# Optimization experiments

Hardware: AMD Instinct MI355X
Metric: run time of the kernel (lower is better)

Reference implementation:

```python
import jax, jax.numpy as jnp
import numpy as np

B = 128
IN = 256
NLVL = 6
KLVL = 3
CH = 4
C = 4 * CH * CH          # 64 channels per node
OU = 8                   # out_filter_siz_u
OV = 8                   # out_filter_siz_v
NK = 2 ** KLVL           # 8 leaf nodes per axis
W_SCALE = 1.0 / 16.0     # ~1/sqrt(2*2*C) so 7 stacked relu-convs stay numerically sane


def setup_inputs() -> dict:
    key = jax.random.key(0)
    ks = jax.random.split(key, 2 * NLVL + 4)
    fx = IN // 2 ** NLVL  # 4: input patch filter size
    inp = {}
    inp["in_data"] = jax.random.normal(ks[0], (B, IN, IN, 1), jnp.float32)
    inp["in_filter"] = jax.random.normal(ks[1], (fx, fx, 1, C), jnp.float32) * W_SCALE
    inp["in_bias"] = jnp.zeros((C,), jnp.float32)
    i = 2
    for lvl in range(1, NLVL + 1):
        n = 2 ** min(lvl, KLVL)  # node grid: grows to 2^klvl then stays
        inp[f"f{lvl}"] = jax.random.normal(ks[i], (n, n, 2, 2, C, C), jnp.float32) * W_SCALE
        inp[f"b{lvl}"] = jnp.zeros((n, n, C), jnp.float32)
        i += 1
    inp["Wd"] = jax.random.normal(ks[i], (NK, NK, 2, C, OU * OV), jnp.float32) * W_SCALE
    return inp


def _node_conv(x, w, b):
    # x: [Nu,Nv,B,H,W,C]; w: [Nu,Nv,2,2,C,C]; 2x2 stride-2 VALID conv per node
    Nu, Nv, Bn, H, W, Cc = x.shape
    xr = x.reshape(Nu, Nv, Bn, H // 2, 2, W // 2, 2, Cc)
    y = jnp.einsum('uvbhxwyc,uvxyco->uvbhwo', xr, w)
    return jax.nn.relu(y + b[:, :, None, None, None, :])


def _forward(in_data, in_filter, in_bias, fs, bs, Wd):
    Bn = in_data.shape[0]
    fx, fy = in_filter.shape[0], in_filter.shape[1]
    # input interp conv: stride == kernel -> non-overlapping patch GEMM
    xr = in_data[..., 0].reshape(Bn, in_data.shape[1] // fx, fx, in_data.shape[2] // fy, fy)
    x = jax.nn.relu(jnp.einsum('bxpyq,pqc->bxyc', xr, in_filter[:, :, 0, :]) + in_bias)
    x = x[None, None]  # [1,1,B,2^nlvl,2^nlvl,C] node grid
    for lvl in range(1, NLVL + 1):
        if lvl <= KLVL:
            # children (itu,itv) read parent (itu//2, itv//2)
            x = jnp.repeat(jnp.repeat(x, 2, axis=0), 2, axis=1)
        x = _node_conv(x, fs[lvl - 1], bs[lvl - 1])
    feats = x[:, :, :, 0, 0, :]  # [NK,NK,B,C]; spatial is 1x1 at level nlvl
    out = jnp.einsum('uvbc,uvrck->uvbrk', feats, Wd)  # r in {real, imag}
    out = out.reshape(NK, NK, Bn, 2, OU, OV)
    out = jnp.transpose(out, (2, 0, 4, 1, 5, 3))  # [B,itu,ou,itv,ov,2]
    return out.reshape(Bn, NK * OU, NK * OV, 2)


def reference(in_data, in_filter, in_bias, f1, b1, f2, b2, f3, b3, f4, b4, f5, b5, f6, b6, Wd):
    fs = (f1, f2, f3, f4, f5, f6)
    bs = (b1, b2, b3, b4, b5, b6)
    return _forward(in_data, in_filter, in_bias, fs, bs, Wd)
```

## Files before the change

kernel.cpp:

```cpp
#include <hip/hip_runtime.h>
#include <hip/hip_bf16.h>
#include <cstdint>
#include <cstddef>


typedef __attribute__((ext_vector_type(8))) short short8;
typedef __attribute__((ext_vector_type(4))) float f32x4;
typedef unsigned short ushort_t;

static __device__ __forceinline__ float b2f(const __hip_bfloat16 x) {
    return __bfloat162float(x);
}
static __device__ __forceinline__ ushort_t f2bf(float x) {
    __hip_bfloat16 h = __float2bfloat16(x);
    ushort_t u;
    __builtin_memcpy(&u, &h, 2);
    return u;
}
static __device__ __forceinline__ void gl_lds16(const void* g, void* l) {
    __builtin_amdgcn_global_load_lds(
        (const __attribute__((address_space(1))) void*)g,
        (__attribute__((address_space(3))) void*)l, 16, 0, 0);
}

#define PREP_BLOCKS 2533

static __device__ __forceinline__ void prep_work(
    int gid, int isbf,
    const void* f1, const void* f2, const void* f3,
    const void* f4, const void* f5, const void* f6, const void* wdsrc,
    const void* b1, const void* b2, const void* b3,
    const void* b4, const void* b5, const void* b6,
    ushort_t* __restrict__ wbuf, ushort_t* __restrict__ wdbuf,
    float* __restrict__ bbuf)
{
    if (gid >= 648448) return;
    if (gid >= 630784) {
        const int bg = gid - 630784;
        const void* src; int base;
        if      (bg <   256) { src = b1; base = 0;     }
        else if (bg <  1280) { src = b2; base = 256;   }
        else if (bg <  5376) { src = b3; base = 1280;  }
        else if (bg <  9472) { src = b4; base = 5376;  }
        else if (bg < 13568) { src = b5; base = 9472;  }
        else                 { src = b6; base = 13568; }
        const int local = bg - base;
        bbuf[bg] = isbf ? b2f(((const __hip_bfloat16*)src)[local])
                        : ((const float*)src)[local];
        return;
    }
    if (gid >= 565248) {
        const int local = gid - 565248;
        const int lane = local & 63;
        const int slot = (local >> 6) & 15;
        const int site = local >> 10;
        const int ks2 = slot >> 3, nh = slot & 7, q = lane >> 4;
        const int n = nh * 16 + (lane & 15);
        const int r = n >> 6, kk = n & 63;
        const int cbase = ks2 * 32 + q * 8;
        ushort_t pk[8];
        if (isbf) {
            const ushort_t* s = (const ushort_t*)wdsrc;
            #pragma unroll
            for (int j = 0; j < 8; j++)
                pk[j] = s[(((size_t)(site * 2 + r) * 64 + cbase + j) * 64) + kk];
        } else {
            const float* s = (const float*)wdsrc;
            #pragma unroll
            for (int j = 0; j < 8; j++)
                pk[j] = f2bf(s[(((size_t)(site * 2 + r) * 64 + cbase + j) * 64) + kk]);
        }
        *(uint4*)&wdbuf[(size_t)local * 8] = *(uint4*)pk;
        return;
    }
    const void* fsrc; int base;
    if      (gid <   8192) { fsrc = f1; base = 0;      }
    else if (gid <  40960) { fsrc = f2; base = 8192;   }
    else if (gid < 172032) { fsrc = f3; base = 40960;  }
    else if (gid < 303104) { fsrc = f4; base = 172032; }
    else if (gid < 434176) { fsrc = f5; base = 303104; }
    else                   { fsrc = f6; base = 434176; }
    const int local = gid - base;
    const int lane = local & 63;
    const int slot = (local >> 6) & 7;
    const int sitetap = local >> 9;
    const int ks = slot >> 2, nh = slot & 3, q = lane >> 4;
    const int n = (lane & 15) + nh * 16;
    const int kbase = ks * 32 + q * 8;
    ushort_t pk[8];
    if (isbf) {
        const ushort_t* s = (const ushort_t*)fsrc + (size_t)sitetap * 4096;
        #pragma unroll
        for (int j = 0; j < 8; j++) pk[j] = s[(kbase + j) * 64 + n];
    } else {
        const float* s = (const float*)fsrc + (size_t)sitetap * 4096;
        #pragma unroll
        for (int j = 0; j < 8; j++) pk[j] = f2bf(s[(kbase + j) * 64 + n]);
    }
    *(uint4*)&wbuf[(size_t)gid * 8] = *(uint4*)pk;
}

static __device__ __forceinline__ void stage0_body(
    int blk, int isbf,
    const void* __restrict__ in_data, const void* __restrict__ filt,
    const void* __restrict__ bias, __hip_bfloat16* __restrict__ x0,
    int b_off)
{
    const int X  = blk & 63;
    const int bl = blk >> 6;
    const int bg = bl + b_off;

    __shared__ float sIn[4][256];
    __shared__ float sF[16][64];
    __shared__ float sB[64];

    const int t = threadIdx.x;
    const size_t srow = ((size_t)bg * 256 + (size_t)X * 4) * 256;

    if (isbf) {
        const __hip_bfloat16* src = (const __hip_bfloat16*)in_data + srow;
        #pragma unroll
        for (int i = 0; i < 4; i++) {
            int flat = i * 256 + t;
            int p = flat >> 8, col = flat & 255;
            sIn[p][col] = b2f(src[(size_t)p * 256 + col]);
        }
        const __hip_bfloat16* fsrc = (const __hip_bfloat16*)filt;
        #pragma unroll
        for (int i = 0; i < 4; i++) {
            int flat = i * 256 + t;
            sF[flat >> 6][flat & 63] = b2f(fsrc[flat]);
        }
        if (t < 64) sB[t] = b2f(((const __hip_bfloat16*)bias)[t]);
    } else {
        const float* src = (const float*)in_data + srow;
        const int p = t >> 6, c4 = (t & 63) * 4;
        *(float4*)&sIn[p][c4] = *(const float4*)(src + (size_t)p * 256 + c4);
        const float* fsrc = (const float*)filt;
        #pragma unroll
        for (int i = 0; i < 4; i++) {
            int flat = i * 256 + t;
            sF[flat >> 6][flat & 63] = fsrc[flat];
        }
        if (t < 64) sB[t] = ((const float*)bias)[t];
    }
    __syncthreads();

    const int ty = t >> 4;
    const int tc = t & 15;

    float acc[4][4];
    {
        const float4 bv = *(const float4*)&sB[tc * 4];
        #pragma unroll
        for (int yi = 0; yi < 4; yi++) {
            acc[yi][0] = bv.x; acc[yi][1] = bv.y;
            acc[yi][2] = bv.z; acc[yi][3] = bv.w;
        }
    }

    #pragma unroll
    for (int p = 0; p < 4; p++) {
        float4 rin[4], rf[4];
        #pragma unroll
        for (int yi = 0; yi < 4; yi++)
            rin[yi] = *(const float4*)&sIn[p][ty * 16 + yi * 4];
        #pragma unroll
        for (int q = 0; q < 4; q++)
            rf[q] = *(const float4*)&sF[p * 4 + q][tc * 4];
        #pragma unroll
        for (int yi = 0; yi < 4; yi++) {
            #pragma unroll
            for (int q = 0; q < 4; q++) {
                const float a = ((const float*)&rin[yi])[q];
                acc[yi][0] = fmaf(a, rf[q].x, acc[yi][0]);
                acc[yi][1] = fmaf(a, rf[q].y, acc[yi][1]);
                acc[yi][2] = fmaf(a, rf[q].z, acc[yi][2]);
                acc[yi][3] = fmaf(a, rf[q].w, acc[yi][3]);
            }
        }
    }

    ushort_t* dst = (ushort_t*)(x0 + ((size_t)bl * 64 + X) * 64 * 64);
    #pragma unroll
    for (int yi = 0; yi < 4; yi++) {
        uint2 pk;
        pk.x = (uint32_t)f2bf(fmaxf(acc[yi][0], 0.f))
             | ((uint32_t)f2bf(fmaxf(acc[yi][1], 0.f)) << 16);
        pk.y = (uint32_t)f2bf(fmaxf(acc[yi][2], 0.f))
             | ((uint32_t)f2bf(fmaxf(acc[yi][3], 0.f)) << 16);
        *(uint2*)(dst + (size_t)(ty * 4 + yi) * 64 + tc * 4) = pk;
    }
}

__global__ __launch_bounds__(256) void k_prep0(
    const void* __restrict__ in_data,
    const void* f1, const void* f2, const void* f3,
    const void* f4, const void* f5, const void* f6, const void* wdsrc,
    const void* b1, const void* b2, const void* b3,
    const void* b4, const void* b5, const void* b6,
    ushort_t* __restrict__ wbuf, ushort_t* __restrict__ wdbuf,
    float* __restrict__ bbuf, int* __restrict__ flag,
    const void* __restrict__ filt, const void* __restrict__ bias0,
    __hip_bfloat16* __restrict__ x0)
{
    __shared__ int sflag;
    const int t = threadIdx.x;
    if (t < 64) {
        const float v = __uint_as_float(((const uint32_t*)in_data)[t]);
        const bool plaus = (v == 0.0f) || (fabsf(v) > 1e-8f && fabsf(v) < 1e4f);
        const unsigned long long m = __ballot(plaus);
        if (t == 0) sflag = (__popcll(m) >= 48) ? 0 : 1;
    }
    __syncthreads();
    const int isbf = sflag;

    if (blockIdx.x < PREP_BLOCKS) {
        if (blockIdx.x == 0 && t == 0) *flag = isbf;
        prep_work(blockIdx.x * 256 + t, isbf,
                  f1, f2, f3, f4, f5, f6, wdsrc,
                  b1, b2, b3, b4, b5, b6, wbuf, wdbuf, bbuf);
    } else {
        stage0_body(blockIdx.x - PREP_BLOCKS, isbf, in_data, filt, bias0, x0, 0);
    }
}

__global__ __launch_bounds__(256) void k_stage0(
    const void* __restrict__ in_data, const void* __restrict__ filt,
    const void* __restrict__ bias, __hip_bfloat16* __restrict__ x0,
    const int* __restrict__ flag, int b_off)
{
    stage0_body(blockIdx.x, *flag, in_data, filt, bias, x0, b_off);
}

__global__ __launch_bounds__(256) void k_level_reg(
    const __hip_bfloat16* __restrict__ xin,
    const ushort_t* __restrict__ wbuf,
    const float* __restrict__ bbuf,
    __hip_bfloat16* __restrict__ xout,
    int Nv_out, int HW, int Bc, int mtiles)
{
    __shared__ ushort_t smem[17408];

    int idx = blockIdx.x;
    const int mt = idx % mtiles; idx /= mtiles;
    const int w  = idx % HW; idx /= HW;
    const int h  = idx % HW; idx /= HW;
    const int Nv_in = Nv_out >> 1;
    const int vp = idx % Nv_in;
    const int up = idx / Nv_in;

    const int t = threadIdx.x;
    const int wave = t >> 6, lane = t & 63;
    const int lm = lane & 15, lq = lane >> 4;

    const int so = (2 * up + (wave >> 1)) * Nv_out + (2 * vp + (wave & 1));
    const int H_in = HW * 2;
    const size_t bstride = (size_t)H_in * H_in * 64;
    const size_t siteb = (size_t)(up * Nv_in + vp) * Bc * bstride;
    const ushort_t* wsite = wbuf + (size_t)so * 4 * 4096 + lane * 8;

    float bv[4];
    #pragma unroll
    for (int fn = 0; fn < 4; fn++) bv[fn] = bbuf[so * 64 + fn * 16 + lm];

    {
        const int hi = 2 * h + (wave >> 1), wi = 2 * w + (wave & 1);
        const size_t tapoff = siteb + ((size_t)hi * H_in + wi) * 64;
        #pragma unroll
        for (int s2 = 0; s2 < 8; s2++) {
            const int ks = s2 >> 2, mh = s2 & 3;
            int b = mt * 64 + mh * 16 + lm;
            if (b >= Bc) b = Bc - 1;
            gl_lds16(xin + tapoff + (size_t)b * bstride + ks * 32 + lq * 8,
                     &smem[(wave * 8 + s2) * 512]);
        }
    }
    __syncthreads();

    const f32x4 zero = {0.f, 0.f, 0.f, 0.f};
    f32x4 acc[4][4];
    #pragma unroll
    for (int i = 0; i < 4; i++)
        #pragma unroll
        for (int j = 0; j < 4; j++) acc[i][j] = zero;

    #pragma unroll
    for (int tap = 0; tap < 4; tap++) {
        short8 B[8];
        #pragma unroll
        for (int s = 0; s < 8; s++)
            B[s] = *(const short8*)(wsite + (tap * 8 + s) * 512);
        #pragma unroll
        for (int ks = 0; ks < 2; ks++) {
            #pragma unroll
            for (int fm = 0; fm < 4; fm++) {
                short8 a = *(const short8*)&smem[(tap * 8 + ks * 4 + fm) * 512 + lane * 8];
                #pragma unroll
                for (int fn = 0; fn < 4; fn++)
                    acc[fm][fn] = __builtin_amdgcn_mfma_f32_16x16x32_bf16(
                        a, B[ks * 4 + fn], acc[fm][fn], 0, 0, 0);
            }
        }
    }
    __syncthreads();

    ushort_t* so_buf = smem + wave * 4352;
    #pragma unroll
    for (int fm = 0; fm < 4; fm++) {
        #pragma unroll
        for (int fn = 0; fn < 4; fn++) {
            #pragma unroll
            for (int r = 0; r < 4; r++) {
                const int row = fm * 16 + lq * 4 + r;
                so_buf[row * 68 + fn * 16 + lm] =
                    f2bf(fmaxf(acc[fm][fn][r] + bv[fn], 0.f));
            }
        }
    }
    __syncthreads();

    const size_t ostride = (size_t)HW * HW * 64;
    const size_t obase = (size_t)so * Bc * ostride + ((size_t)h * HW + w) * 64;
    #pragma unroll
    for (int i = 0; i < 8; i++) {
        const int task = i * 64 + lane;
        const int oct = task & 7, row = task >> 3;
        const int b = mt * 64 + row;
        if (b < Bc) {
            *(uint4*)(xout + obase + (size_t)b * ostride + oct * 8) =
                *(const uint4*)&so_buf[row * 68 + oct * 8];
        }
    }
}

__global__ __launch_bounds__(256, 1) void k_f456(
    const __hip_bfloat16* __restrict__ xin,
    const ushort_t* __restrict__ w4, const ushort_t* __restrict__ w5,
    const ushort_t* __restrict__ w6, const ushort_t* __restrict__ wd,
    const float* __restrict__ b4, const float* __restrict__ b5,
    const float* __restrict__ b6,
    void* __restrict__ out, const int* __restrict__ flag,
    int Bc, int b_off, int mtiles)
{
    const int isbf = *flag;
    const int bx = blockIdx.x;
    const int mt = bx % mtiles;
    const int site = bx / mtiles;
    const int u = site >> 3, v = site & 7;

    __shared__ ushort_t smem[36096];

    const int t = threadIdx.x;
    const int wv = t >> 6, lane = t & 63;
    const int lm = lane & 15, lq = lane >> 4;

    const ushort_t* w4s = w4 + (size_t)site * 16384 + lane * 8;
    const ushort_t* w5s = w5 + (size_t)site * 16384 + lane * 8;
    const ushort_t* w6s = w6 + (size_t)site * 16384 + lane * 8;
    const ushort_t* wds = wd + (size_t)site * 8192  + lane * 8;

    float bv4[4], bv5[4];
    #pragma unroll
    for (int fn = 0; fn < 4; fn++) {
        bv4[fn] = b4[site * 64 + fn * 16 + lm];
        bv5[fn] = b5[site * 64 + fn * 16 + lm];
    }
    const float bv6 = b6[site * 64 + wv * 16 + lm];

    const f32x4 zero = {0.f, 0.f, 0.f, 0.f};
    const int h5 = wv >> 1, w5p = wv & 1;
    ushort_t* mid1w = smem + wv * 8448;
    const size_t sb = (size_t)site * Bc;

    int brow[2];
    #pragma unroll
    for (int mh = 0; mh < 2; mh++) {
        int b = mt * 32 + mh * 16 + lm;
        if (b >= Bc) b = Bc - 1;
        brow[mh] = b;
    }
    const __hip_bfloat16* xbase0 = xin + (sb + brow[0]) * 4096 + lq * 8;
    const __hip_bfloat16* xbase1 = xin + (sb + brow[1]) * 4096 + lq * 8;

    for (int i = 0; i < 4; i++) {
        const int h4 = 2 * h5 + (i >> 1), w4p = 2 * w5p + (i & 1);
        f32x4 acc[2][4];
        #pragma unroll
        for (int a_ = 0; a_ < 2; a_++)
            #pragma unroll
            for (int b_ = 0; b_ < 4; b_++) acc[a_][b_] = zero;

        #pragma unroll
        for (int tap = 0; tap < 4; tap++) {
            const int h3 = 2 * h4 + (tap >> 1), w3 = 2 * w4p + (tap & 1);
            const int poff = (h3 * 8 + w3) * 64;
            #pragma unroll
            for (int ks = 0; ks < 2; ks++) {
                short8 a0 = *(const short8*)(xbase0 + poff + ks * 32);
                short8 a1 = *(const short8*)(xbase1 + poff + ks * 32);
                #pragma unroll
                for (int fn = 0; fn < 4; fn++) {
                    short8 bfr = *(const short8*)(w4s + (tap * 8 + ks * 4 + fn) * 512);
                    acc[0][fn] = __builtin_amdgcn_mfma_f32_16x16x32_bf16(a0, bfr, acc[0][fn], 0, 0, 0);
                    acc[1][fn] = __builtin_amdgcn_mfma_f32_16x16x32_bf16(a1, bfr, acc[1][fn], 0, 0, 0);
                }
            }
        }
        #pragma unroll
        for (int fm = 0; fm < 2; fm++) {
            #pragma unroll
            for (int fn = 0; fn < 4; fn++) {
                #pragma unroll
                for (int r = 0; r < 4; r++) {
                    const int m = fm * 16 + lq * 4 + r;
                    const int ch = fn * 16 + lm;
                    mid1w[m * 264 + i * 64 + ch] =
                        f2bf(fmaxf(acc[fm][fn][r] + bv4[fn], 0.f));
                }
            }
        }
    }

    {
        f32x4 acc2[2][4];
        #pragma unroll
        for (int a_ = 0; a_ < 2; a_++)
            #pragma unroll
            for (int b_ = 0; b_ < 4; b_++) acc2[a_][b_] = zero;

        #pragma unroll
        for (int i = 0; i < 4; i++) {
            #pragma unroll
            for (int ks = 0; ks < 2; ks++) {
                short8 a0 = *(const short8*)&mid1w[lm * 264 + i * 64 + ks * 32 + lq * 8];
                short8 a1 = *(const short8*)&mid1w[(16 + lm) * 264 + i * 64 + ks * 32 + lq * 8];
                #pragma unroll
                for (int fn = 0; fn < 4; fn++) {
                    short8 bfr = *(const short8*)(w5s + (i * 8 + ks * 4 + fn) * 512);
                    acc2[0][fn] = __builtin_amdgcn_mfma_f32_16x16x32_bf16(a0, bfr, acc2[0][fn], 0, 0, 0);
                    acc2[1][fn] = __builtin_amdgcn_mfma_f32_16x16x32_bf16(a1, bfr, acc2[1][fn], 0, 0, 0);
                }
            }
        }
        #pragma unroll
        for (int fm = 0; fm < 2; fm++) {
            #pragma unroll
            for (int fn = 0; fn < 4; fn++) {
                #pragma unroll
                for (int r = 0; r < 4; r++) {
                    const int m = fm * 16 + lq * 4 + r;
                    const int ch = fn * 16 + lm;
                    mid1w[m * 72 + ch] =
                        f2bf(fmaxf(acc2[fm][fn][r] + bv5[fn], 0.f));
                }
            }
        }
    }
    __syncthreads();

    {
        f32x4 acc3[2];
        acc3[0] = zero; acc3[1] = zero;
        #pragma unroll
        for (int tap = 0; tap < 4; tap++) {
            const ushort_t* sl = smem + tap * 8448;
            #pragma unroll
            for (int ks = 0; ks < 2; ks++) {
                short8 a0 = *(const short8*)&sl[lm * 72 + ks * 32 + lq * 8];
                short8 a1 = *(const short8*)&sl[(16 + lm) * 72 + ks * 32 + lq * 8];
                short8 bfr = *(const short8*)(w6s + (tap * 8 + ks * 4 + wv) * 512);
                acc3[0] = __builtin_amdgcn_mfma_f32_16x16x32_bf16(a0, bfr, acc3[0], 0, 0, 0);
                acc3[1] = __builtin_amdgcn_mfma_f32_16x16x32_bf16(a1, bfr, acc3[1], 0, 0, 0);
            }
        }
        ushort_t* mid3 = smem + 33792;
        #pragma unroll
        for (int fm = 0; fm < 2; fm++) {
            #pragma unroll
            for (int r = 0; r < 4; r++) {
                const int m = fm * 16 + lq * 4 + r;
                const int ch = wv * 16 + lm;
                mid3[m * 72 + ch] =
                    f2bf(fmaxf(acc3[fm][r] + bv6, 0.f));
            }
        }
    }
    __syncthreads();

    {
        const ushort_t* mid3 = smem + 33792;
        f32x4 acc4[2][2];
        acc4[0][0] = zero; acc4[0][1] = zero; acc4[1][0] = zero; acc4[1][1] = zero;
        #pragma unroll
        for (int ks = 0; ks < 2; ks++) {
            short8 a0 = *(const short8*)&mid3[lm * 72 + ks * 32 + lq * 8];
            short8 a1 = *(const short8*)&mid3[(16 + lm) * 72 + ks * 32 + lq * 8];
            #pragma unroll
            for (int n2 = 0; n2 < 2; n2++) {
                const int nh = 2 * wv + n2;
                short8 bfr = *(const short8*)(wds + (ks * 8 + nh) * 512);
                acc4[0][n2] = __builtin_amdgcn_mfma_f32_16x16x32_bf16(a0, bfr, acc4[0][n2], 0, 0, 0);
                acc4[1][n2] = __builtin_amdgcn_mfma_f32_16x16x32_bf16(a1, bfr, acc4[1][n2], 0, 0, 0);
            }
        }
        #pragma unroll
        for (int fm = 0; fm < 2; fm++) {
            #pragma unroll
            for (int n2 = 0; n2 < 2; n2++) {
                const int n = (2 * wv + n2) * 16 + lm;
                const int rr = n >> 6, ou = (n >> 3) & 7, ov = n & 7;
                const size_t obase =
                    (((size_t)(u * 8 + ou)) * 64 + (v * 8 + ov)) * 2 + rr;
                #pragma unroll
                for (int reg = 0; reg < 4; reg++) {
                    const int brw = mt * 32 + fm * 16 + lq * 4 + reg;
                    if (brw < Bc) {
                        const size_t oidx = obase + (size_t)(b_off + brw) * 8192;
                        if (isbf) ((__hip_bfloat16*)out)[oidx] =
                            __float2bfloat16(acc4[fm][n2][reg]);
                        else ((float*)out)[oidx] = acc4[fm][n2][reg];
                    }
                }
            }
        }
    }
}

extern "C" void kernel_launch(void* const* d_in, const int* in_sizes, int n_in,
                              void* d_out, int out_size, void* d_ws, size_t ws_size,
                              hipStream_t stream)
{
    (void)in_sizes; (void)n_in; (void)out_size;

    const void* in_data = d_in[0];
    const void* filt    = d_in[1];
    const void* bias0   = d_in[2];
    const void* fl[7];
    const void* bl[7];
    for (int l = 1; l <= 6; l++) {
        fl[l] = d_in[1 + 2 * l];
        bl[l] = d_in[2 + 2 * l];
    }
    const void* Wd = d_in[15];

    const int Bfull = 128;
    const size_t perB = (size_t)64 * 64 * 64;

    const size_t wbufBytes  = 565248ull * 16;
    const size_t wdbufBytes = 65536ull * 16;
    const size_t bbufBytes  = 17664ull * 4;
    const size_t headBytes  = 256 + wbufBytes + wdbufBytes + bbufBytes;

    const size_t avail = ws_size > headBytes ? ws_size - headBytes : 0;
    int Bc = 0;
    for (int c = 128; c >= 1; c >>= 1) {
        if ((size_t)2 * c * perB * sizeof(__hip_bfloat16) <= avail) { Bc = c; break; }
    }
    if (Bc == 0) return;

    int* flag = (int*)d_ws;
    ushort_t* wbuf  = (ushort_t*)((char*)d_ws + 256);
    ushort_t* wdbuf = (ushort_t*)((char*)d_ws + 256 + wbufBytes);
    float* bbuf = (float*)((char*)d_ws + 256 + wbufBytes + wdbufBytes);
    __hip_bfloat16* bufA = (__hip_bfloat16*)((char*)d_ws + headBytes);
    __hip_bfloat16* bufB = bufA + (size_t)Bc * perB;

    static const size_t w_off[7] = {0, 0, 65536, 327680, 1376256, 2424832, 3473408};
    static const int    b_off_tab[7] = {0, 0, 256, 1280, 5376, 9472, 13568};

    const int mt4 = (Bc + 63) / 64;
    const int mt32 = (Bc + 31) / 32;

    for (int b_off = 0; b_off < Bfull; b_off += Bc) {
        if (b_off == 0) {
            k_prep0<<<dim3(PREP_BLOCKS + Bc * 64), 256, 0, stream>>>(
                in_data,
                fl[1], fl[2], fl[3], fl[4], fl[5], fl[6], Wd,
                bl[1], bl[2], bl[3], bl[4], bl[5], bl[6],
                wbuf, wdbuf, bbuf, flag,
                filt, bias0, bufA);
        } else {
            k_stage0<<<dim3(Bc * 64), 256, 0, stream>>>(in_data, filt, bias0, bufA, flag, b_off);
        }

        __hip_bfloat16* cur = bufA;
        __hip_bfloat16* nxt = bufB;
        for (int lvl = 1; lvl <= 3; lvl++) {
            const int Nu = 1 << lvl;
            const int H  = 64 >> lvl;
            const int Nv_in = Nu >> 1;
            dim3 grid(Nv_in * Nv_in * H * H * mt4);
            k_level_reg<<<grid, 256, 0, stream>>>(cur, wbuf + w_off[lvl],
                bbuf + b_off_tab[lvl], nxt, Nu, H, Bc, mt4);
            __hip_bfloat16* tmp = cur; cur = nxt; nxt = tmp;
        }

        k_f456<<<dim3(64 * mt32), 256, 0, stream>>>(cur,
            wbuf + w_off[4], wbuf + w_off[5], wbuf + w_off[6], wdbuf,
            bbuf + b_off_tab[4], bbuf + b_off_tab[5], bbuf + b_off_tab[6],
            d_out, flag, Bc, b_off, mt32);
    }
}
```

Measured before the change: 279.6 us.

## Restructure level kernels to stream per-tap tiles and weights through LDS

The level kernel now loops over the four taps, staging one tap's activation tile and all four child-sites' weights into LDS per iteration, instead of loading all taps up front and reading weights straight from global into registers. The fused levels 4-6 kernel stages w4/w5 into shared memory, shrinks its batch tile from 32 to 16 rows (doubling the grid), drops the single-block occupancy bound, and prefetches w6/Wd fragments into registers early. The aim is to cut scattered global weight loads and raise parallelism, at the cost of extra barriers per tap, more LDS traffic, and the level-4-6 weights being reloaded by twice as many blocks.

```diff
diff --git a/kernel.cpp b/kernel.cpp
--- a/kernel.cpp
+++ b/kernel.cpp
@@ -22,6 +22,8 @@
         (const __attribute__((address_space(1))) void*)g,
         (__attribute__((address_space(3))) void*)l, 16, 0, 0);
 }
+#define WAIT_LGKM0() __builtin_amdgcn_s_waitcnt(0xC07F)
+#define WAIT_VM0()   __builtin_amdgcn_s_waitcnt(0x0F70)
 
 #define PREP_BLOCKS 2533
 
@@ -233,14 +235,17 @@
     stage0_body(blockIdx.x, *flag, in_data, filt, bias, x0, b_off);
 }
 
-__global__ __launch_bounds__(256) void k_level_reg(
+__global__ __launch_bounds__(256) void k_level4(
     const __hip_bfloat16* __restrict__ xin,
     const ushort_t* __restrict__ wbuf,
     const float* __restrict__ bbuf,
     __hip_bfloat16* __restrict__ xout,
     int Nv_out, int HW, int Bc, int mtiles)
 {
-    __shared__ ushort_t smem[17408];
+    __shared__ ushort_t smem[20480];
+    __shared__ float sBias[4][64];
+    ushort_t* sA = smem;
+    ushort_t* sB = smem + 4096;
 
     int idx = blockIdx.x;
     const int mt = idx % mtiles; idx /= mtiles;
@@ -254,29 +259,17 @@
     const int wave = t >> 6, lane = t & 63;
     const int lm = lane & 15, lq = lane >> 4;
 
+    {
+        const int ct = t >> 6, o = t & 63;
+        const int so_t = (2 * up + (ct >> 1)) * Nv_out + (2 * vp + (ct & 1));
+        sBias[ct][o] = bbuf[so_t * 64 + o];
+    }
+
     const int so = (2 * up + (wave >> 1)) * Nv_out + (2 * vp + (wave & 1));
     const int H_in = HW * 2;
     const size_t bstride = (size_t)H_in * H_in * 64;
     const size_t siteb = (size_t)(up * Nv_in + vp) * Bc * bstride;
-    const ushort_t* wsite = wbuf + (size_t)so * 4 * 4096 + lane * 8;
-
-    float bv[4];
-    #pragma unroll
-    for (int fn = 0; fn < 4; fn++) bv[fn] = bbuf[so * 64 + fn * 16 + lm];
-
-    {
-        const int hi = 2 * h + (wave >> 1), wi = 2 * w + (wave & 1);
-        const size_t tapoff = siteb + ((size_t)hi * H_in + wi) * 64;
-        #pragma unroll
-        for (int s2 = 0; s2 < 8; s2++) {
-            const int ks = s2 >> 2, mh = s2 & 3;
-            int b = mt * 64 + mh * 16 + lm;
-            if (b >= Bc) b = Bc - 1;
-            gl_lds16(xin + tapoff + (size_t)b * bstride + ks * 32 + lq * 8,
-                     &smem[(wave * 8 + s2) * 512]);
-        }
-    }
-    __syncthreads();
+    const ushort_t* wsite = wbuf + (size_t)so * 4 * 4096;
 
     const f32x4 zero = {0.f, 0.f, 0.f, 0.f};
     f32x4 acc[4][4];
@@ -285,26 +278,46 @@
         #pragma unroll
         for (int j = 0; j < 4; j++) acc[i][j] = zero;
 
+    for (int tap = 0; tap < 4; tap++) {
+        const int hi = 2 * h + (tap >> 1), wi = 2 * w + (tap & 1);
+        const size_t tapoff = siteb + ((size_t)hi * H_in + wi) * 64;
+        #pragma unroll
+        for (int s2 = 0; s2 < 2; s2++) {
+            const int s = wave * 2 + s2;
+            const int ks = s >> 2, mh = s & 3;
+            int b = mt * 64 + lm + mh * 16;
+            if (b >= Bc) b = Bc - 1;
+            gl_lds16(xin + tapoff + (size_t)b * bstride + ks * 32 + lq * 8,
+                     &sA[s * 512]);
+        }
+        const ushort_t* wt = wsite + (size_t)tap * 4096;
+        #pragma unroll
+        for (int s = 0; s < 8; s++) {
+            gl_lds16(wt + s * 512 + lane * 8, &sB[wave * 4096 + s * 512]);
+        }
+        __syncthreads();
+
+        #pragma unroll
+        for (int ks = 0; ks < 2; ks++) {
+            short8 bf0 = *(const short8*)&sB[wave * 4096 + (ks * 4 + 0) * 512 + lane * 8];
+            short8 bf1 = *(const short8*)&sB[wave * 4096 + (ks * 4 + 1) * 512 + lane * 8];
+            short8 bf2 = *(const short8*)&sB[wave * 4096 + (ks * 4 + 2) * 512 + lane * 8];
+            short8 bf3 = *(const short8*)&sB[wave * 4096 + (ks * 4 + 3) * 512 + lane * 8];
+            #pragma unroll
+            for (int fm = 0; fm < 4; fm++) {
+                short8 a = *(const short8*)&sA[(ks * 4 + fm) * 512 + lane * 8];
+                acc[fm][0] = __builtin_amdgcn_mfma_f32_16x16x32_bf16(a, bf0, acc[fm][0], 0, 0, 0);
+                acc[fm][1] = __builtin_amdgcn_mfma_f32_16x16x32_bf16(a, bf1, acc[fm][1], 0, 0, 0);
+                acc[fm][2] = __builtin_amdgcn_mfma_f32_16x16x32_bf16(a, bf2, acc[fm][2], 0, 0, 0);
+                acc[fm][3] = __builtin_amdgcn_mfma_f32_16x16x32_bf16(a, bf3, acc[fm][3], 0, 0, 0);
+            }
+        }
+        __syncthreads();
+    }
+
+    float bv[4];
     #pragma unroll
-    for (int tap = 0; tap < 4; tap++) {
-        short8 B[8];
-        #pragma unroll
-        for (int s = 0; s < 8; s++)
-            B[s] = *(const short8*)(wsite + (tap * 8 + s) * 512);
-        #pragma unroll
-        for (int ks = 0; ks < 2; ks++) {
-            #pragma unroll
-            for (int fm = 0; fm < 4; fm++) {
-                short8 a = *(const short8*)&smem[(tap * 8 + ks * 4 + fm) * 512 + lane * 8];
-                #pragma unroll
-                for (int fn = 0; fn < 4; fn++)
-                    acc[fm][fn] = __builtin_amdgcn_mfma_f32_16x16x32_bf16(
-                        a, B[ks * 4 + fn], acc[fm][fn], 0, 0, 0);
-            }
-        }
-    }
-    __syncthreads();
-
+    for (int fn = 0; fn < 4; fn++) bv[fn] = sBias[wave][fn * 16 + lm];
     ushort_t* so_buf = smem + wave * 4352;
     #pragma unroll
     for (int fm = 0; fm < 4; fm++) {
@@ -334,7 +347,7 @@
     }
 }
 
-__global__ __launch_bounds__(256, 1) void k_f456(
+__global__ __launch_bounds__(256) void k_f456(
     const __hip_bfloat16* __restrict__ xin,
     const ushort_t* __restrict__ w4, const ushort_t* __restrict__ w5,
     const ushort_t* __restrict__ w6, const ushort_t* __restrict__ wd,
@@ -349,14 +362,12 @@
     const int site = bx / mtiles;
     const int u = site >> 3, v = site & 7;
 
-    __shared__ ushort_t smem[36096];
+    __shared__ ushort_t smem[37376];
 
     const int t = threadIdx.x;
     const int wv = t >> 6, lane = t & 63;
     const int lm = lane & 15, lq = lane >> 4;
 
-    const ushort_t* w4s = w4 + (size_t)site * 16384 + lane * 8;
-    const ushort_t* w5s = w5 + (size_t)site * 16384 + lane * 8;
     const ushort_t* w6s = w6 + (size_t)site * 16384 + lane * 8;
     const ushort_t* wds = wd + (size_t)site * 8192  + lane * 8;
 
@@ -368,159 +379,166 @@
     }
     const float bv6 = b6[site * 64 + wv * 16 + lm];
 
+    {
+        const ushort_t* w4s = w4 + (size_t)site * 16384;
+        #pragma unroll
+        for (int s2 = 0; s2 < 8; s2++) {
+            const int s = wv * 8 + s2;
+            gl_lds16(w4s + s * 512 + lane * 8, &smem[s * 512]);
+        }
+    }
+    __syncthreads();
+
     const f32x4 zero = {0.f, 0.f, 0.f, 0.f};
     const int h5 = wv >> 1, w5p = wv & 1;
-    ushort_t* mid1w = smem + wv * 8448;
+    ushort_t* mid1w = smem + 16384 + wv * 4224;
+    ushort_t* Aw = smem + 33280 + wv * 1024;
     const size_t sb = (size_t)site * Bc;
 
-    int brow[2];
-    #pragma unroll
-    for (int mh = 0; mh < 2; mh++) {
-        int b = mt * 32 + mh * 16 + lm;
-        if (b >= Bc) b = Bc - 1;
-        brow[mh] = b;
-    }
-    const __hip_bfloat16* xbase0 = xin + (sb + brow[0]) * 4096 + lq * 8;
-    const __hip_bfloat16* xbase1 = xin + (sb + brow[1]) * 4096 + lq * 8;
+    int brow = mt * 16 + lm;
+    if (brow >= Bc) brow = Bc - 1;
+    const __hip_bfloat16* xbase = xin + (sb + brow) * 4096 + lq * 8;
 
     for (int i = 0; i < 4; i++) {
         const int h4 = 2 * h5 + (i >> 1), w4p = 2 * w5p + (i & 1);
-        f32x4 acc[2][4];
-        #pragma unroll
-        for (int a_ = 0; a_ < 2; a_++)
-            #pragma unroll
-            for (int b_ = 0; b_ < 4; b_++) acc[a_][b_] = zero;
-
-        #pragma unroll
+        f32x4 acc[4];
+        #pragma unroll
+        for (int b_ = 0; b_ < 4; b_++) acc[b_] = zero;
+
         for (int tap = 0; tap < 4; tap++) {
             const int h3 = 2 * h4 + (tap >> 1), w3 = 2 * w4p + (tap & 1);
             const int poff = (h3 * 8 + w3) * 64;
+            WAIT_LGKM0();
             #pragma unroll
             for (int ks = 0; ks < 2; ks++) {
-                short8 a0 = *(const short8*)(xbase0 + poff + ks * 32);
-                short8 a1 = *(const short8*)(xbase1 + poff + ks * 32);
+                gl_lds16(xbase + poff + ks * 32, &Aw[ks * 512]);
+            }
+            WAIT_VM0();
+            __builtin_amdgcn_sched_barrier(0);
+            #pragma unroll
+            for (int ks = 0; ks < 2; ks++) {
+                short8 a = *(const short8*)&Aw[ks * 512 + lane * 8];
                 #pragma unroll
                 for (int fn = 0; fn < 4; fn++) {
-                    short8 bfr = *(const short8*)(w4s + (tap * 8 + ks * 4 + fn) * 512);
-                    acc[0][fn] = __builtin_amdgcn_mfma_f32_16x16x32_bf16(a0, bfr, acc[0][fn], 0, 0, 0);
-                    acc[1][fn] = __builtin_amdgcn_mfma_f32_16x16x32_bf16(a1, bfr, acc[1][fn], 0, 0, 0);
+                    short8 bfr = *(const short8*)&smem[(tap * 8 + ks * 4 + fn) * 512 + lane * 8];
+                    acc[fn] = __builtin_amdgcn_mfma_f32_16x16x32_bf16(a, bfr, acc[fn], 0, 0, 0);
                 }
             }
         }
         #pragma unroll
-        for (int fm = 0; fm < 2; fm++) {
-            #pragma unroll
-            for (int fn = 0; fn < 4; fn++) {
-                #pragma unroll
-                for (int r = 0; r < 4; r++) {
-                    const int m = fm * 16 + lq * 4 + r;
-                    const int ch = fn * 16 + lm;
-                    mid1w[m * 264 + i * 64 + ch] =
-                        f2bf(fmaxf(acc[fm][fn][r] + bv4[fn], 0.f));
-                }
-            }
-        }
-    }
+        for (int fn = 0; fn < 4; fn++) {
+            #pragma unroll
+            for (int r = 0; r < 4; r++) {
+                const int m = lq * 4 + r;
+                const int ch = fn * 16 + lm;
+                mid1w[m * 264 + i * 64 + ch] =
+                    f2bf(fmaxf(acc[fn][r] + bv4[fn], 0.f));
+            }
+        }
+    }
+    __syncthreads();
 
     {
-        f32x4 acc2[2][4];
-        #pragma unroll
-        for (int a_ = 0; a_ < 2; a_++)
-            #pragma unroll
-            for (int b_ = 0; b_ < 4; b_++) acc2[a_][b_] = zero;
+        const ushort_t* w5s = w5 + (size_t)site * 16384;
+        #pragma unroll
+        for (int s2 = 0; s2 < 8; s2++) {
+            const int s = wv * 8 + s2;
+            gl_lds16(w5s + s * 512 + lane * 8, &smem[s * 512]);
+        }
+    }
+    __syncthreads();
+
+    short8 b3r[8];
+    short8 wdr[4];
+    {
+        f32x4 acc2[4];
+        #pragma unroll
+        for (int b_ = 0; b_ < 4; b_++) acc2[b_] = zero;
 
         #pragma unroll
         for (int i = 0; i < 4; i++) {
             #pragma unroll
             for (int ks = 0; ks < 2; ks++) {
                 short8 a0 = *(const short8*)&mid1w[lm * 264 + i * 64 + ks * 32 + lq * 8];
-                short8 a1 = *(const short8*)&mid1w[(16 + lm) * 264 + i * 64 + ks * 32 + lq * 8];
                 #pragma unroll
                 for (int fn = 0; fn < 4; fn++) {
-                    short8 bfr = *(const short8*)(w5s + (i * 8 + ks * 4 + fn) * 512);
-                    acc2[0][fn] = __builtin_amdgcn_mfma_f32_16x16x32_bf16(a0, bfr, acc2[0][fn], 0, 0, 0);
-                    acc2[1][fn] = __builtin_amdgcn_mfma_f32_16x16x32_bf16(a1, bfr, acc2[1][fn], 0, 0, 0);
+                    short8 bfr = *(const short8*)&smem[(i * 8 + ks * 4 + fn) * 512 + lane * 8];
+                    acc2[fn] = __builtin_amdgcn_mfma_f32_16x16x32_bf16(a0, bfr, acc2[fn], 0, 0, 0);
                 }
             }
         }
-        #pragma unroll
-        for (int fm = 0; fm < 2; fm++) {
-            #pragma unroll
-            for (int fn = 0; fn < 4; fn++) {
-                #pragma unroll
-                for (int r = 0; r < 4; r++) {
-                    const int m = fm * 16 + lq * 4 + r;
-                    const int ch = fn * 16 + lm;
-                    mid1w[m * 72 + ch] =
-                        f2bf(fmaxf(acc2[fm][fn][r] + bv5[fn], 0.f));
-                }
+
+        #pragma unroll
+        for (int tap = 0; tap < 4; tap++)
+            #pragma unroll
+            for (int ks = 0; ks < 2; ks++)
+                b3r[tap * 2 + ks] = *(const short8*)(w6s + (tap * 8 + ks * 4 + wv) * 512);
+        #pragma unroll
+        for (int ks = 0; ks < 2; ks++)
+            #pragma unroll
+            for (int n2 = 0; n2 < 2; n2++)
+                wdr[ks * 2 + n2] = *(const short8*)(wds + (ks * 8 + 2 * wv + n2) * 512);
+
+        #pragma unroll
+        for (int fn = 0; fn < 4; fn++) {
+            #pragma unroll
+            for (int r = 0; r < 4; r++) {
+                const int m = lq * 4 + r;
+                const int ch = fn * 16 + lm;
+                mid1w[m * 72 + ch] =
+                    f2bf(fmaxf(acc2[fn][r] + bv5[fn], 0.f));
             }
         }
     }
     __syncthreads();
 
     {
-        f32x4 acc3[2];
-        acc3[0] = zero; acc3[1] = zero;
+        f32x4 acc3 = zero;
         #pragma unroll
         for (int tap = 0; tap < 4; tap++) {
-            const ushort_t* sl = smem + tap * 8448;
+            const ushort_t* sl = smem + 16384 + tap * 4224;
             #pragma unroll
             for (int ks = 0; ks < 2; ks++) {
                 short8 a0 = *(const short8*)&sl[lm * 72 + ks * 32 + lq * 8];
-                short8 a1 = *(const short8*)&sl[(16 + lm) * 72 + ks * 32 + lq * 8];
-                short8 bfr = *(const short8*)(w6s + (tap * 8 + ks * 4 + wv) * 512);
-                acc3[0] = __builtin_amdgcn_mfma_f32_16x16x32_bf16(a0, bfr, acc3[0], 0, 0, 0);
-                acc3[1] = __builtin_amdgcn_mfma_f32_16x16x32_bf16(a1, bfr, acc3[1], 0, 0, 0);
-            }
-        }
-        ushort_t* mid3 = smem + 33792;
-        #pragma unroll
-        for (int fm = 0; fm < 2; fm++) {
-            #pragma unroll
-            for (int r = 0; r < 4; r++) {
-                const int m = fm * 16 + lq * 4 + r;
-                const int ch = wv * 16 + lm;
-                mid3[m * 72 + ch] =
-                    f2bf(fmaxf(acc3[fm][r] + bv6, 0.f));
-            }
+                acc3 = __builtin_amdgcn_mfma_f32_16x16x32_bf16(a0, b3r[tap * 2 + ks], acc3, 0, 0, 0);
+            }
+        }
+        ushort_t* mid3 = smem + 33280;
+        #pragma unroll
+        for (int r = 0; r < 4; r++) {
+            const int m = lq * 4 + r;
+            const int ch = wv * 16 + lm;
+            mid3[m * 72 + ch] = f2bf(fmaxf(acc3[r] + bv6, 0.f));
         }
     }
     __syncthreads();
 
     {
-        const ushort_t* mid3 = smem + 33792;
-        f32x4 acc4[2][2];
-        acc4[0][0] = zero; acc4[0][1] = zero; acc4[1][0] = zero; acc4[1][1] = zero;
+        const ushort_t* mid3 = smem + 33280;
+        f32x4 acc4[2];
+        acc4[0] = zero; acc4[1] = zero;
         #pragma unroll
         for (int ks = 0; ks < 2; ks++) {
             short8 a0 = *(const short8*)&mid3[lm * 72 + ks * 32 + lq * 8];
-            short8 a1 = *(const short8*)&mid3[(16 + lm) * 72 + ks * 32 + lq * 8];
             #pragma unroll
             for (int n2 = 0; n2 < 2; n2++) {
-                const int nh = 2 * wv + n2;
-                short8 bfr = *(const short8*)(wds + (ks * 8 + nh) * 512);
-                acc4[0][n2] = __builtin_amdgcn_mfma_f32_16x16x32_bf16(a0, bfr, acc4[0][n2], 0, 0, 0);
-                acc4[1][n2] = __builtin_amdgcn_mfma_f32_16x16x32_bf16(a1, bfr, acc4[1][n2], 0, 0, 0);
-            }
-        }
-        #pragma unroll
-        for (int fm = 0; fm < 2; fm++) {
-            #pragma unroll
-            for (int n2 = 0; n2 < 2; n2++) {
-                const int n = (2 * wv + n2) * 16 + lm;
-                const int rr = n >> 6, ou = (n >> 3) & 7, ov = n & 7;
-                const size_t obase =
-                    (((size_t)(u * 8 + ou)) * 64 + (v * 8 + ov)) * 2 + rr;
-                #pragma unroll
-                for (int reg = 0; reg < 4; reg++) {
-                    const int brw = mt * 32 + fm * 16 + lq * 4 + reg;
-                    if (brw < Bc) {
-                        const size_t oidx = obase + (size_t)(b_off + brw) * 8192;
-                        if (isbf) ((__hip_bfloat16*)out)[oidx] =
-                            __float2bfloat16(acc4[fm][n2][reg]);
-                        else ((float*)out)[oidx] = acc4[fm][n2][reg];
-                    }
+                acc4[n2] = __builtin_amdgcn_mfma_f32_16x16x32_bf16(a0, wdr[ks * 2 + n2], acc4[n2], 0, 0, 0);
+            }
+        }
+        #pragma unroll
+        for (int n2 = 0; n2 < 2; n2++) {
+            const int n = (2 * wv + n2) * 16 + lm;
+            const int rr = n >> 6, ou = (n >> 3) & 7, ov = n & 7;
+            const size_t obase =
+                (((size_t)(u * 8 + ou)) * 64 + (v * 8 + ov)) * 2 + rr;
+            #pragma unroll
+            for (int reg = 0; reg < 4; reg++) {
+                const int brw = mt * 16 + lq * 4 + reg;
+                if (brw < Bc) {
+                    const size_t oidx = obase + (size_t)(b_off + brw) * 8192;
+                    if (isbf) ((__hip_bfloat16*)out)[oidx] =
+                        __float2bfloat16(acc4[n2][reg]);
+                    else ((float*)out)[oidx] = acc4[n2][reg];
                 }
             }
         }
@@ -570,7 +588,7 @@
     static const int    b_off_tab[7] = {0, 0, 256, 1280, 5376, 9472, 13568};
 
     const int mt4 = (Bc + 63) / 64;
-    const int mt32 = (Bc + 31) / 32;
+    const int mt16 = (Bc + 15) / 16;
 
     for (int b_off = 0; b_off < Bfull; b_off += Bc) {
         if (b_off == 0) {
@@ -591,14 +609,14 @@
             const int H  = 64 >> lvl;
             const int Nv_in = Nu >> 1;
             dim3 grid(Nv_in * Nv_in * H * H * mt4);
-            k_level_reg<<<grid, 256, 0, stream>>>(cur, wbuf + w_off[lvl],
+            k_level4<<<grid, 256, 0, stream>>>(cur, wbuf + w_off[lvl],
                 bbuf + b_off_tab[lvl], nxt, Nu, H, Bc, mt4);
             __hip_bfloat16* tmp = cur; cur = nxt; nxt = tmp;
         }
 
-        k_f456<<<dim3(64 * mt32), 256, 0, stream>>>(cur,
+        k_f456<<<dim3(64 * mt16), 256, 0, stream>>>(cur,
             wbuf + w_off[4], wbuf + w_off[5], wbuf + w_off[6], wdbuf,
             bbuf + b_off_tab[4], bbuf + b_off_tab[5], bbuf + b_off_tab[6],
-            d_out, flag, Bc, b_off, mt32);
-    }
-}
+            d_out, flag, Bc, b_off, mt16);
+    }
+}
```

Result: faster. 249.6 us (-10.7%).
